# Kernel tuning notes

Hardware: AMD Instinct MI355X
Metric: run time of the kernel (lower is better)

The kernel has to match this reference:

```python
import jax, jax.numpy as jnp
import numpy as np

B, S, D, H = 2, 2048, 768, 12
DK = D // H


def setup_inputs() -> dict:
    key = jax.random.key(0)
    ks = jax.random.split(key, 10)
    sc = 0.02
    return {
        "k": jax.random.normal(ks[0], (B, S, D), jnp.float32),
        "q": jax.random.normal(ks[1], (B, S, D), jnp.float32),
        "v": jax.random.normal(ks[2], (B, S, D), jnp.float32),
        "mask": jnp.ones((B, 1, S, S), jnp.int32),
        "wq": jax.random.normal(ks[3], (D, D), jnp.float32) * sc,
        "bq": jnp.zeros((D,), jnp.float32),
        "wk": jax.random.normal(ks[4], (D, D), jnp.float32) * sc,
        "bk": jnp.zeros((D,), jnp.float32),
        "wv": jax.random.normal(ks[5], (D, D), jnp.float32) * sc,
        "bv": jnp.zeros((D,), jnp.float32),
        "wo": jax.random.normal(ks[6], (D, D), jnp.float32) * sc,
        "bo": jnp.zeros((D,), jnp.float32),
    }


def reference(k, q, v, mask, wq, bq, wk, bk, wv, bv, wo, bo):
    # Linear projections (torch Linear: x @ W^T + b)
    query = q @ wq.T + bq
    key_ = k @ wk.T + bk
    value = v @ wv.T + bv
    # [B,S,D] -> [B,H,S,DK]
    def split_heads(x):
        return x.reshape(B, S, H, DK).transpose(0, 2, 1, 3)
    Q, K, V = split_heads(query), split_heads(key_), split_heads(value)
    # NOTE: original masked_fill result is discarded -> mask is a no-op.
    scores = jnp.einsum("bhqd,bhkd->bhqk", Q, K) / jnp.sqrt(jnp.float32(DK))
    attn = jax.nn.softmax(scores, axis=-1)  # dropout p=0.0 -> identity
    out = jnp.einsum("bhqk,bhkd->bhqd", attn, V)
    out = out.transpose(0, 2, 1, 3).reshape(B, S, D)
    return out @ wo.T + bo
```

## Files before the change

### kernel.cpp

```cpp
#include <hip/hip_runtime.h>
#include <hip/hip_bf16.h>

#define B_  2
#define S_  2048
#define D_  768
#define H_  12
#define DK_ 64
#define NX_ (B_*S_*D_)
#define NW_ (D_*D_)

typedef __attribute__((ext_vector_type(8))) short  bf16x8;
typedef __attribute__((ext_vector_type(4))) float  f32x4;

__device__ __forceinline__ unsigned short f2bf(float f) {
    unsigned int u = __float_as_uint(f);
    u += 0x7fffu + ((u >> 16) & 1u);
    return (unsigned short)(u >> 16);
}

__device__ __forceinline__ void async_cp16(const unsigned short* g,
                                           const unsigned short* lds_uniform_base) {
    __builtin_amdgcn_global_load_lds(
        (const __attribute__((address_space(1))) unsigned int*)(uintptr_t)g,
        (__attribute__((address_space(3))) unsigned int*)(unsigned int)(uintptr_t)lds_uniform_base,
        16, 0, 0);
}

struct CvtArgs { const float* s[7]; unsigned short* d[7]; };

__global__ __launch_bounds__(256) void cvt_kernel(CvtArgs a) {
    const int reg = blockIdx.y;
    const int n = (reg < 3) ? NX_ : NW_;
    const long i = ((long)blockIdx.x * 256 + threadIdx.x) * 8;
    if (i >= n) return;
    const float4 f0 = *(const float4*)(a.s[reg] + i);
    const float4 f1 = *(const float4*)(a.s[reg] + i + 4);
    unsigned short o[8] = {f2bf(f0.x), f2bf(f0.y), f2bf(f0.z), f2bf(f0.w),
                           f2bf(f1.x), f2bf(f1.y), f2bf(f1.z), f2bf(f1.w)};
    *(uint4*)(a.d[reg] + i) = *(const uint4*)o;
}

struct QkvArgs {
    const unsigned short* A[3];
    const unsigned short* W[3];
    const float* bias[3];
    unsigned short* out[3];
};

__global__ __launch_bounds__(256) void gemm_qkv(QkvArgs args, int zoff) {
    __shared__ unsigned short smem[12288];
    unsigned short* As = smem;
    unsigned short* Bs = smem + 8192;

    const int t    = threadIdx.x;
    const int wave = t >> 6;
    const int lane = t & 63;
    const int l16  = lane & 15;
    const int quad = lane >> 4;
    const int m0   = blockIdx.x * 128;
    const int head = blockIdx.y;
    const int n0   = head * 64;
    const int zz   = blockIdx.z + zoff;

    const unsigned short* Ap = args.A[zz];
    const unsigned short* Wp = args.W[zz];

    f32x4 acc[2][4];
#pragma unroll
    for (int s = 0; s < 2; s++)
#pragma unroll
        for (int j = 0; j < 4; j++) acc[s][j] = (f32x4){0.f, 0.f, 0.f, 0.f};

    const int lrow = lane >> 3;
    const int lcg  = (lane & 7) * 8;

    for (int k0 = 0; k0 < D_; k0 += 64) {
#pragma unroll
        for (int i = 0; i < 4; i++) {
            const int chunk = wave * 4 + i;
            async_cp16(Ap + (long)(m0 + chunk * 8 + lrow) * D_ + k0 + lcg,
                       As + chunk * 512);
        }
#pragma unroll
        for (int i = 0; i < 2; i++) {
            const int chunk = wave * 2 + i;
            async_cp16(Wp + (long)(n0 + chunk * 8 + lrow) * D_ + k0 + lcg,
                       Bs + chunk * 512);
        }
        __syncthreads();
#pragma unroll
        for (int ks = 0; ks < 2; ks++) {
            bf16x8 af[2];
#pragma unroll
            for (int s = 0; s < 2; s++)
                af[s] = *(const bf16x8*)&As[(wave * 32 + s * 16 + l16) * 64 + ks * 32 + quad * 8];
#pragma unroll
            for (int j = 0; j < 4; j++) {
                const bf16x8 bf = *(const bf16x8*)&Bs[(j * 16 + l16) * 64 + ks * 32 + quad * 8];
#pragma unroll
                for (int s = 0; s < 2; s++)
                    acc[s][j] = __builtin_amdgcn_mfma_f32_16x16x32_bf16(af[s], bf, acc[s][j], 0, 0, 0);
            }
        }
        __syncthreads();
    }

    const int b     = m0 >> 11;
    const int sbase = m0 & (S_ - 1);
    float bv4[4];
#pragma unroll
    for (int j = 0; j < 4; j++) bv4[j] = args.bias[zz][n0 + j * 16 + l16];

    if (zz < 2) {
        unsigned short* Op = args.out[zz] + (long)(b * H_ + head) * S_ * DK_;
#pragma unroll
        for (int s = 0; s < 2; s++)
#pragma unroll
            for (int j = 0; j < 4; j++)
#pragma unroll
                for (int r = 0; r < 4; r++) {
                    const int srow = sbase + wave * 32 + s * 16 + quad * 4 + r;
                    Op[(long)srow * DK_ + j * 16 + l16] = f2bf(acc[s][j][r] + bv4[j]);
                }
    } else {
        unsigned short* Ls = smem;
#pragma unroll
        for (int s = 0; s < 2; s++)
#pragma unroll
            for (int j = 0; j < 4; j++)
#pragma unroll
                for (int r = 0; r < 4; r++)
                    Ls[(j * 16 + l16) * 136 + wave * 32 + s * 16 + quad * 4 + r] =
                        f2bf(acc[s][j][r] + bv4[j]);
        __syncthreads();
        const int dk = t >> 2;
        const int sg = (t & 3) * 32;
        uint4 w0 = *(const uint4*)&Ls[dk * 136 + sg];
        uint4 w1 = *(const uint4*)&Ls[dk * 136 + sg + 8];
        uint4 w2 = *(const uint4*)&Ls[dk * 136 + sg + 16];
        uint4 w3 = *(const uint4*)&Ls[dk * 136 + sg + 24];
        unsigned short* Op = args.out[2] +
            ((long)(b * H_ + head) * DK_ + dk) * S_ + sbase + sg;
        *(uint4*)(Op)      = w0;
        *(uint4*)(Op + 8)  = w1;
        *(uint4*)(Op + 16) = w2;
        *(uint4*)(Op + 24) = w3;
    }
}

__global__ __launch_bounds__(256) void attn_kernel(
    const unsigned short* __restrict__ Q, const unsigned short* __restrict__ K,
    const unsigned short* __restrict__ Vt, unsigned short* __restrict__ O)
{
    const int t    = threadIdx.x;
    const int wave = t >> 6;
    const int lane = t & 63;
    const int l16  = lane & 15;
    const int quad = lane >> 4;
    const int qtile = blockIdx.x;
    const int bh    = blockIdx.y;

    const unsigned short* Qp = Q  + (long)bh * S_ * DK_;
    const unsigned short* Kp = K  + (long)bh * S_ * DK_;
    const unsigned short* Vp = Vt + (long)bh * DK_ * S_;

    __shared__ unsigned short Ks[2][64 * 72];
    __shared__ unsigned short Vs[2][64 * 72];
    __shared__ unsigned short Ps[64 * 72];

    bf16x8 qfrag[2];
    {
        const long qoff = (long)(qtile * 64 + wave * 16 + l16) * DK_ + quad * 8;
        qfrag[0] = *(const bf16x8*)(Qp + qoff);
        qfrag[1] = *(const bf16x8*)(Qp + qoff + 32);
    }

    const int srow = t >> 3;
    const int scg  = (t & 7) * 8;
    uint4 kreg[2], vreg[2];

    kreg[0] = *(const uint4*)(Kp + (long)srow * DK_ + scg);
    kreg[1] = *(const uint4*)(Kp + (long)(srow + 32) * DK_ + scg);
    vreg[0] = *(const uint4*)(Vp + (long)srow * S_ + scg);
    vreg[1] = *(const uint4*)(Vp + (long)(srow + 32) * S_ + scg);
    *(uint4*)&Ks[0][srow * 72 + scg]        = kreg[0];
    *(uint4*)&Ks[0][(srow + 32) * 72 + scg] = kreg[1];
    *(uint4*)&Vs[0][srow * 72 + scg]        = vreg[0];
    *(uint4*)&Vs[0][(srow + 32) * 72 + scg] = vreg[1];
    __syncthreads();

    f32x4 oacc[4];
#pragma unroll
    for (int j = 0; j < 4; j++) oacc[j] = (f32x4){0.f, 0.f, 0.f, 0.f};
    float lsum[4] = {0.f, 0.f, 0.f, 0.f};

    const float C = 0.18033688011112042f;

    for (int it = 0; it < 32; ++it) {
        const int cur = it & 1;
        if (it < 31) {
            const int kv0 = (it + 1) * 64;
            kreg[0] = *(const uint4*)(Kp + (long)(kv0 + srow) * DK_ + scg);
            kreg[1] = *(const uint4*)(Kp + (long)(kv0 + srow + 32) * DK_ + scg);
            vreg[0] = *(const uint4*)(Vp + (long)srow * S_ + kv0 + scg);
            vreg[1] = *(const uint4*)(Vp + (long)(srow + 32) * S_ + kv0 + scg);
        }

        f32x4 sacc[4];
#pragma unroll
        for (int j = 0; j < 4; j++) sacc[j] = (f32x4){0.f, 0.f, 0.f, 0.f};
#pragma unroll
        for (int ks = 0; ks < 2; ks++)
#pragma unroll
            for (int j = 0; j < 4; j++) {
                const bf16x8 bf = *(const bf16x8*)&Ks[cur][(j * 16 + l16) * 72 + ks * 32 + quad * 8];
                sacc[j] = __builtin_amdgcn_mfma_f32_16x16x32_bf16(qfrag[ks], bf, sacc[j], 0, 0, 0);
            }

#pragma unroll
        for (int j = 0; j < 4; j++)
#pragma unroll
            for (int r = 0; r < 4; r++) {
                const float p = exp2f(sacc[j][r] * C);
                lsum[r] += p;
                Ps[(wave * 16 + quad * 4 + r) * 72 + j * 16 + l16] = f2bf(p);
            }

#pragma unroll
        for (int ks = 0; ks < 2; ks++) {
            const bf16x8 pf = *(const bf16x8*)&Ps[(wave * 16 + l16) * 72 + ks * 32 + quad * 8];
#pragma unroll
            for (int j = 0; j < 4; j++) {
                const bf16x8 vf = *(const bf16x8*)&Vs[cur][(j * 16 + l16) * 72 + ks * 32 + quad * 8];
                oacc[j] = __builtin_amdgcn_mfma_f32_16x16x32_bf16(pf, vf, oacc[j], 0, 0, 0);
            }
        }

        if (it < 31) {
            const int nxt = cur ^ 1;
            *(uint4*)&Ks[nxt][srow * 72 + scg]        = kreg[0];
            *(uint4*)&Ks[nxt][(srow + 32) * 72 + scg] = kreg[1];
            *(uint4*)&Vs[nxt][srow * 72 + scg]        = vreg[0];
            *(uint4*)&Vs[nxt][(srow + 32) * 72 + scg] = vreg[1];
        }
        __syncthreads();
    }

#pragma unroll
    for (int r = 0; r < 4; r++) {
#pragma unroll
        for (int off = 1; off < 16; off <<= 1)
            lsum[r] += __shfl_xor(lsum[r], off, 64);
        lsum[r] = 1.f / lsum[r];
    }

    const int b = bh / H_, h = bh % H_;
#pragma unroll
    for (int j = 0; j < 4; j++)
#pragma unroll
        for (int r = 0; r < 4; r++) {
            const int qrow = qtile * 64 + wave * 16 + quad * 4 + r;
            O[(long)(b * S_ + qrow) * D_ + h * DK_ + j * 16 + l16] =
                f2bf(oacc[j][r] * lsum[r]);
        }
}

__global__ __launch_bounds__(256) void gemm_out(
    const unsigned short* __restrict__ A, const unsigned short* __restrict__ W,
    const float* __restrict__ bias, float* __restrict__ Out)
{
    __shared__ unsigned short smem[12288];
    unsigned short* As = smem;
    unsigned short* Bs = smem + 8192;

    const int t    = threadIdx.x;
    const int wave = t >> 6;
    const int lane = t & 63;
    const int l16  = lane & 15;
    const int quad = lane >> 4;
    const int m0   = blockIdx.x * 128;
    const int n0   = blockIdx.y * 64;

    f32x4 acc[2][4];
#pragma unroll
    for (int s = 0; s < 2; s++)
#pragma unroll
        for (int j = 0; j < 4; j++) acc[s][j] = (f32x4){0.f, 0.f, 0.f, 0.f};

    const int lrow = lane >> 3;
    const int lcg  = (lane & 7) * 8;

    for (int k0 = 0; k0 < D_; k0 += 64) {
#pragma unroll
        for (int i = 0; i < 4; i++) {
            const int chunk = wave * 4 + i;
            async_cp16(A + (long)(m0 + chunk * 8 + lrow) * D_ + k0 + lcg,
                       As + chunk * 512);
        }
#pragma unroll
        for (int i = 0; i < 2; i++) {
            const int chunk = wave * 2 + i;
            async_cp16(W + (long)(n0 + chunk * 8 + lrow) * D_ + k0 + lcg,
                       Bs + chunk * 512);
        }
        __syncthreads();
#pragma unroll
        for (int ks = 0; ks < 2; ks++) {
            bf16x8 af[2];
#pragma unroll
            for (int s = 0; s < 2; s++)
                af[s] = *(const bf16x8*)&As[(wave * 32 + s * 16 + l16) * 64 + ks * 32 + quad * 8];
#pragma unroll
            for (int j = 0; j < 4; j++) {
                const bf16x8 bf = *(const bf16x8*)&Bs[(j * 16 + l16) * 64 + ks * 32 + quad * 8];
#pragma unroll
                for (int s = 0; s < 2; s++)
                    acc[s][j] = __builtin_amdgcn_mfma_f32_16x16x32_bf16(af[s], bf, acc[s][j], 0, 0, 0);
            }
        }
        __syncthreads();
    }

#pragma unroll
    for (int j = 0; j < 4; j++) {
        const float bv = bias[n0 + j * 16 + l16];
#pragma unroll
        for (int s = 0; s < 2; s++)
#pragma unroll
            for (int r = 0; r < 4; r++) {
                const int m = m0 + wave * 32 + s * 16 + quad * 4 + r;
                Out[(long)m * D_ + n0 + j * 16 + l16] = acc[s][j][r] + bv;
            }
    }
}

extern "C" void kernel_launch(void* const* d_in, const int* in_sizes, int n_in,
                              void* d_out, int out_size, void* d_ws, size_t ws_size,
                              hipStream_t stream) {
    const float* k_in = (const float*)d_in[0];
    const float* q_in = (const float*)d_in[1];
    const float* v_in = (const float*)d_in[2];
    const float* wq = (const float*)d_in[4];
    const float* bq = (const float*)d_in[5];
    const float* wk = (const float*)d_in[6];
    const float* bk = (const float*)d_in[7];
    const float* wv = (const float*)d_in[8];
    const float* bv = (const float*)d_in[9];
    const float* wo = (const float*)d_in[10];
    const float* bo = (const float*)d_in[11];

    unsigned short* ws = (unsigned short*)d_ws;
    unsigned short* R0 = ws;
    unsigned short* R1 = ws + 1ll * NX_;
    unsigned short* R2 = ws + 2ll * NX_;

    const size_t need_fused = (6ull * NX_ + 4ull * NW_) * 2;
    const bool fused = ws_size >= need_fused;

    unsigned short *Qb, *Kb, *Vtp, *Ao, *Wc;
    if (fused) {
        Qb  = ws + 3ll * NX_;
        Kb  = ws + 4ll * NX_;
        Vtp = ws + 5ll * NX_;
        Ao  = R0;
        Wc  = ws + 6ll * NX_;
    } else {
        Qb  = ws + 3ll * NX_;
        Kb  = R0;
        Vtp = R1;
        Ao  = R2;
        Wc  = ws + 4ll * NX_;
    }
    unsigned short* W0 = Wc;
    unsigned short* W1 = Wc + 1ll * NW_;
    unsigned short* W2 = Wc + 2ll * NW_;
    unsigned short* W3 = Wc + 3ll * NW_;

    CvtArgs ca;
    ca.s[0] = q_in; ca.s[1] = k_in; ca.s[2] = v_in;
    ca.s[3] = wq;   ca.s[4] = wk;   ca.s[5] = wv;  ca.s[6] = wo;
    ca.d[0] = R0;   ca.d[1] = R1;   ca.d[2] = R2;
    ca.d[3] = W0;   ca.d[4] = W1;   ca.d[5] = W2;  ca.d[6] = W3;
    cvt_kernel<<<dim3(NX_ / 2048, 7), 256, 0, stream>>>(ca);

    QkvArgs qa;
    qa.A[0] = R0;  qa.A[1] = R1;  qa.A[2] = R2;
    qa.W[0] = W0;  qa.W[1] = W1;  qa.W[2] = W2;
    qa.bias[0] = bq; qa.bias[1] = bk; qa.bias[2] = bv;
    qa.out[0] = Qb; qa.out[1] = Kb; qa.out[2] = Vtp;

    if (fused) {
        gemm_qkv<<<dim3(32, 12, 3), 256, 0, stream>>>(qa, 0);
    } else {
        gemm_qkv<<<dim3(32, 12, 1), 256, 0, stream>>>(qa, 0);
        gemm_qkv<<<dim3(32, 12, 1), 256, 0, stream>>>(qa, 1);
        gemm_qkv<<<dim3(32, 12, 1), 256, 0, stream>>>(qa, 2);
    }

    attn_kernel<<<dim3(S_ / 64, B_ * H_), 256, 0, stream>>>(Qb, Kb, Vtp, Ao);
    gemm_out<<<dim3(32, 12), 256, 0, stream>>>(Ao, W3, bo, (float*)d_out);
}
```

Baseline: 234.9 us.

## Fuse input conversion into QKV GEMM, split-KV attention, swizzled weights, retile GEMMs

Drops the separate fp32-to-bf16 conversion of the activations and converts them inside the QKV GEMM as they are loaded. Only the weights are still pre-converted, now into an XOR-swizzled LDS-friendly layout. The QKV GEMM moves to 128x128 tiles with a 2x2 wave layout and staged coalesced epilogues. Attention processes 128 query rows per block and splits the KV range in two, with a combine kernel that merges the partial sums. The output GEMM uses smaller 64x64 tiles for more blocks. These changes remove a full pass over the activations and add parallelism, at the cost of extra fp32 partial traffic and an extra launch.

After: 241.4 us. 2.8% more time.

```diff
diff --git a/kernel.cpp b/kernel.cpp
--- a/kernel.cpp
+++ b/kernel.cpp
@@ -8,6 +8,7 @@
 #define DK_ 64
 #define NX_ (B_*S_*D_)
 #define NW_ (D_*D_)
+#define NR_ (B_*H_*S_)
 
 typedef __attribute__((ext_vector_type(8))) short  bf16x8;
 typedef __attribute__((ext_vector_type(4))) float  f32x4;
@@ -26,29 +27,33 @@
         16, 0, 0);
 }
 
-struct CvtArgs { const float* s[7]; unsigned short* d[7]; };
-
-__global__ __launch_bounds__(256) void cvt_kernel(CvtArgs a) {
-    const int reg = blockIdx.y;
-    const int n = (reg < 3) ? NX_ : NW_;
-    const long i = ((long)blockIdx.x * 256 + threadIdx.x) * 8;
-    if (i >= n) return;
-    const float4 f0 = *(const float4*)(a.s[reg] + i);
-    const float4 f1 = *(const float4*)(a.s[reg] + i + 4);
+__global__ __launch_bounds__(256) void cvt_w(const float* __restrict__ w0,
+                                             const float* __restrict__ w1,
+                                             const float* __restrict__ w2,
+                                             const float* __restrict__ w3,
+                                             unsigned short* __restrict__ dst) {
+    const float* src[4] = {w0, w1, w2, w3};
+    const int widx = blockIdx.y;
+    const int idx  = blockIdx.x * 256 + threadIdx.x;
+    const int n = idx / 96;
+    const int g = idx % 96;
+    const float4 f0 = *(const float4*)(src[widx] + (long)n * D_ + g * 8);
+    const float4 f1 = *(const float4*)(src[widx] + (long)n * D_ + g * 8 + 4);
     unsigned short o[8] = {f2bf(f0.x), f2bf(f0.y), f2bf(f0.z), f2bf(f0.w),
                            f2bf(f1.x), f2bf(f1.y), f2bf(f1.z), f2bf(f1.w)};
-    *(uint4*)(a.d[reg] + i) = *(const uint4*)o;
+    const int kdst = (g >> 3) * 64 + (((g & 7) ^ (n & 7)) * 8);
+    *(uint4*)(dst + (long)widx * NW_ + (long)n * D_ + kdst) = *(const uint4*)o;
 }
 
 struct QkvArgs {
-    const unsigned short* A[3];
-    const unsigned short* W[3];
+    const float* X[3];
     const float* bias[3];
     unsigned short* out[3];
 };
 
-__global__ __launch_bounds__(256) void gemm_qkv(QkvArgs args, int zoff) {
-    __shared__ unsigned short smem[12288];
+__global__ __launch_bounds__(256, 2) void gemm_qkv(QkvArgs args,
+                                                   const unsigned short* __restrict__ Wsw) {
+    __shared__ __align__(16) unsigned short smem[17408];
     unsigned short* As = smem;
     unsigned short* Bs = smem + 8192;
 
@@ -57,100 +62,126 @@
     const int lane = t & 63;
     const int l16  = lane & 15;
     const int quad = lane >> 4;
+    const int wm   = wave >> 1, wn = wave & 1;
     const int m0   = blockIdx.x * 128;
-    const int head = blockIdx.y;
-    const int n0   = head * 64;
-    const int zz   = blockIdx.z + zoff;
-
-    const unsigned short* Ap = args.A[zz];
-    const unsigned short* Wp = args.W[zz];
-
-    f32x4 acc[2][4];
-#pragma unroll
-    for (int s = 0; s < 2; s++)
+    const int zz   = blockIdx.y / 6;
+    const int nb   = blockIdx.y % 6;
+    const int n0   = nb * 128;
+
+    const float* Xp = args.X[zz];
+    const unsigned short* Wp = Wsw + (long)zz * NW_;
+
+    f32x4 acc[4][4];
+#pragma unroll
+    for (int s = 0; s < 4; s++)
 #pragma unroll
         for (int j = 0; j < 4; j++) acc[s][j] = (f32x4){0.f, 0.f, 0.f, 0.f};
 
-    const int lrow = lane >> 3;
-    const int lcg  = (lane & 7) * 8;
+    const int arow = t >> 3;
+    const int acg  = t & 7;
+    const int brow = lane >> 3;
+    const int bcg  = lane & 7;
 
     for (int k0 = 0; k0 < D_; k0 += 64) {
+        __syncthreads();
 #pragma unroll
         for (int i = 0; i < 4; i++) {
             const int chunk = wave * 4 + i;
-            async_cp16(Ap + (long)(m0 + chunk * 8 + lrow) * D_ + k0 + lcg,
-                       As + chunk * 512);
-        }
-#pragma unroll
-        for (int i = 0; i < 2; i++) {
-            const int chunk = wave * 2 + i;
-            async_cp16(Wp + (long)(n0 + chunk * 8 + lrow) * D_ + k0 + lcg,
+            async_cp16(Wp + (long)(n0 + chunk * 8 + brow) * D_ + k0 + bcg * 8,
                        Bs + chunk * 512);
         }
+#pragma unroll
+        for (int p = 0; p < 4; p++) {
+            const int r = p * 32 + arow;
+            const float4 f0 = *(const float4*)(Xp + (long)(m0 + r) * D_ + k0 + acg * 8);
+            const float4 f1 = *(const float4*)(Xp + (long)(m0 + r) * D_ + k0 + acg * 8 + 4);
+            unsigned short o[8] = {f2bf(f0.x), f2bf(f0.y), f2bf(f0.z), f2bf(f0.w),
+                                   f2bf(f1.x), f2bf(f1.y), f2bf(f1.z), f2bf(f1.w)};
+            *(uint4*)(As + r * 64 + ((acg ^ (r & 7)) * 8)) = *(const uint4*)o;
+        }
         __syncthreads();
 #pragma unroll
         for (int ks = 0; ks < 2; ks++) {
-            bf16x8 af[2];
-#pragma unroll
-            for (int s = 0; s < 2; s++)
-                af[s] = *(const bf16x8*)&As[(wave * 32 + s * 16 + l16) * 64 + ks * 32 + quad * 8];
+            const int cg = ks * 4 + quad;
+            bf16x8 af[4], bf[4];
+#pragma unroll
+            for (int s = 0; s < 4; s++) {
+                const int r = wm * 64 + s * 16 + l16;
+                af[s] = *(const bf16x8*)&As[r * 64 + ((cg ^ (r & 7)) * 8)];
+            }
 #pragma unroll
             for (int j = 0; j < 4; j++) {
-                const bf16x8 bf = *(const bf16x8*)&Bs[(j * 16 + l16) * 64 + ks * 32 + quad * 8];
-#pragma unroll
-                for (int s = 0; s < 2; s++)
-                    acc[s][j] = __builtin_amdgcn_mfma_f32_16x16x32_bf16(af[s], bf, acc[s][j], 0, 0, 0);
-            }
-        }
-        __syncthreads();
-    }
+                const int r = wn * 64 + j * 16 + l16;
+                bf[j] = *(const bf16x8*)&Bs[r * 64 + ((cg ^ (r & 7)) * 8)];
+            }
+#pragma unroll
+            for (int s = 0; s < 4; s++)
+#pragma unroll
+                for (int j = 0; j < 4; j++)
+                    acc[s][j] = __builtin_amdgcn_mfma_f32_16x16x32_bf16(af[s], bf[j], acc[s][j], 0, 0, 0);
+        }
+    }
+    __syncthreads();
 
     const int b     = m0 >> 11;
     const int sbase = m0 & (S_ - 1);
-    float bv4[4];
-#pragma unroll
-    for (int j = 0; j < 4; j++) bv4[j] = args.bias[zz][n0 + j * 16 + l16];
+    float bv[4];
+#pragma unroll
+    for (int j = 0; j < 4; j++) bv[j] = args.bias[zz][n0 + wn * 64 + j * 16 + l16];
 
     if (zz < 2) {
-        unsigned short* Op = args.out[zz] + (long)(b * H_ + head) * S_ * DK_;
-#pragma unroll
-        for (int s = 0; s < 2; s++)
+        unsigned short* Ls = smem;
+#pragma unroll
+        for (int s = 0; s < 4; s++)
 #pragma unroll
             for (int j = 0; j < 4; j++)
 #pragma unroll
-                for (int r = 0; r < 4; r++) {
-                    const int srow = sbase + wave * 32 + s * 16 + quad * 4 + r;
-                    Op[(long)srow * DK_ + j * 16 + l16] = f2bf(acc[s][j][r] + bv4[j]);
-                }
+                for (int r = 0; r < 4; r++)
+                    Ls[(wm * 64 + s * 16 + quad * 4 + r) * 136 + wn * 64 + j * 16 + l16] =
+                        f2bf(acc[s][j][r] + bv[j]);
+        __syncthreads();
+        const int row  = t >> 1;
+        const int half = t & 1;
+        unsigned short* Op = args.out[zz];
+#pragma unroll
+        for (int i = 0; i < 8; i++) {
+            const int col  = half * 64 + i * 8;
+            const int head = nb * 2 + half;
+            const uint4 v = *(const uint4*)&Ls[row * 136 + col];
+            *(uint4*)(Op + ((long)(b * H_ + head) * S_ + sbase + row) * DK_ + (col & 63)) = v;
+        }
     } else {
         unsigned short* Ls = smem;
 #pragma unroll
-        for (int s = 0; s < 2; s++)
+        for (int s = 0; s < 4; s++)
 #pragma unroll
             for (int j = 0; j < 4; j++)
 #pragma unroll
-                for (int r = 0; r < 4; r++)
-                    Ls[(j * 16 + l16) * 136 + wave * 32 + s * 16 + quad * 4 + r] =
-                        f2bf(acc[s][j][r] + bv4[j]);
-        __syncthreads();
-        const int dk = t >> 2;
-        const int sg = (t & 3) * 32;
-        uint4 w0 = *(const uint4*)&Ls[dk * 136 + sg];
-        uint4 w1 = *(const uint4*)&Ls[dk * 136 + sg + 8];
-        uint4 w2 = *(const uint4*)&Ls[dk * 136 + sg + 16];
-        uint4 w3 = *(const uint4*)&Ls[dk * 136 + sg + 24];
-        unsigned short* Op = args.out[2] +
-            ((long)(b * H_ + head) * DK_ + dk) * S_ + sbase + sg;
-        *(uint4*)(Op)      = w0;
-        *(uint4*)(Op + 8)  = w1;
-        *(uint4*)(Op + 16) = w2;
-        *(uint4*)(Op + 24) = w3;
-    }
-}
-
-__global__ __launch_bounds__(256) void attn_kernel(
+                for (int r = 0; r < 4; r++) {
+                    const int dk  = j * 16 + l16;
+                    const int pos = wm * 64 + (quad * 4 + r) * 4 + s;
+                    Ls[wn * 8704 + dk * 136 + pos] = f2bf(acc[s][j][r] + bv[j]);
+                }
+        __syncthreads();
+        const int rowIdx = t >> 1;
+        const int hh = rowIdx >> 6, dk = rowIdx & 63;
+        const int half = t & 1;
+        unsigned short* Op = args.out[2];
+#pragma unroll
+        for (int i = 0; i < 8; i++) {
+            const int col = half * 64 + i * 8;
+            const uint4 v = *(const uint4*)&Ls[hh * 8704 + dk * 136 + col];
+            const int head = nb * 2 + hh;
+            *(uint4*)(Op + ((long)(b * H_ + head) * DK_ + dk) * S_ + sbase + col) = v;
+        }
+    }
+}
+
+__global__ __launch_bounds__(256, 3) void attn_kernel(
     const unsigned short* __restrict__ Q, const unsigned short* __restrict__ K,
-    const unsigned short* __restrict__ Vt, unsigned short* __restrict__ O)
+    const unsigned short* __restrict__ Vt,
+    float* __restrict__ Opart, float* __restrict__ Lp,
+    unsigned short* __restrict__ Ao, int kvlen, int direct)
 {
     const int t    = threadIdx.x;
     const int wave = t >> 6;
@@ -159,177 +190,238 @@
     const int quad = lane >> 4;
     const int qtile = blockIdx.x;
     const int bh    = blockIdx.y;
+    const int z     = blockIdx.z;
+    const int kvbase = z * kvlen;
+    const int NIT    = kvlen >> 6;
 
     const unsigned short* Qp = Q  + (long)bh * S_ * DK_;
     const unsigned short* Kp = K  + (long)bh * S_ * DK_;
     const unsigned short* Vp = Vt + (long)bh * DK_ * S_;
 
-    __shared__ unsigned short Ks[2][64 * 72];
-    __shared__ unsigned short Vs[2][64 * 72];
-    __shared__ unsigned short Ps[64 * 72];
-
-    bf16x8 qfrag[2];
+    __shared__ __align__(16) unsigned short smem[18432];
+    unsigned short* Ks = smem;
+    unsigned short* Vs = smem + 4608;
+    unsigned short* Ps = smem + 9216;
+
+    bf16x8 qfrag[2][2];
+#pragma unroll
+    for (int st = 0; st < 2; st++) {
+        const long qoff = (long)(qtile * 128 + wave * 32 + st * 16 + l16) * DK_ + quad * 8;
+        qfrag[st][0] = *(const bf16x8*)(Qp + qoff);
+        qfrag[st][1] = *(const bf16x8*)(Qp + qoff + 32);
+    }
+
+    const int srow = t >> 2;
+    const int scg  = (t & 3) * 16;
+    uint4 kreg[2], vreg[2];
     {
-        const long qoff = (long)(qtile * 64 + wave * 16 + l16) * DK_ + quad * 8;
-        qfrag[0] = *(const bf16x8*)(Qp + qoff);
-        qfrag[1] = *(const bf16x8*)(Qp + qoff + 32);
-    }
-
-    const int srow = t >> 3;
-    const int scg  = (t & 7) * 8;
-    uint4 kreg[2], vreg[2];
-
-    kreg[0] = *(const uint4*)(Kp + (long)srow * DK_ + scg);
-    kreg[1] = *(const uint4*)(Kp + (long)(srow + 32) * DK_ + scg);
-    vreg[0] = *(const uint4*)(Vp + (long)srow * S_ + scg);
-    vreg[1] = *(const uint4*)(Vp + (long)(srow + 32) * S_ + scg);
-    *(uint4*)&Ks[0][srow * 72 + scg]        = kreg[0];
-    *(uint4*)&Ks[0][(srow + 32) * 72 + scg] = kreg[1];
-    *(uint4*)&Vs[0][srow * 72 + scg]        = vreg[0];
-    *(uint4*)&Vs[0][(srow + 32) * 72 + scg] = vreg[1];
-    __syncthreads();
-
-    f32x4 oacc[4];
-#pragma unroll
-    for (int j = 0; j < 4; j++) oacc[j] = (f32x4){0.f, 0.f, 0.f, 0.f};
-    float lsum[4] = {0.f, 0.f, 0.f, 0.f};
+        const unsigned short* gk = Kp + (long)(kvbase + srow) * DK_ + scg;
+        const unsigned short* gv = Vp + (long)srow * S_ + kvbase + scg;
+        kreg[0] = *(const uint4*)gk;  kreg[1] = *(const uint4*)(gk + 8);
+        vreg[0] = *(const uint4*)gv;  vreg[1] = *(const uint4*)(gv + 8);
+    }
+
+    f32x4 oacc[2][4];
+#pragma unroll
+    for (int st = 0; st < 2; st++)
+#pragma unroll
+        for (int j = 0; j < 4; j++) oacc[st][j] = (f32x4){0.f, 0.f, 0.f, 0.f};
+    float lsum[2][4] = {{0.f,0.f,0.f,0.f},{0.f,0.f,0.f,0.f}};
 
     const float C = 0.18033688011112042f;
 
-    for (int it = 0; it < 32; ++it) {
-        const int cur = it & 1;
-        if (it < 31) {
-            const int kv0 = (it + 1) * 64;
-            kreg[0] = *(const uint4*)(Kp + (long)(kv0 + srow) * DK_ + scg);
-            kreg[1] = *(const uint4*)(Kp + (long)(kv0 + srow + 32) * DK_ + scg);
-            vreg[0] = *(const uint4*)(Vp + (long)srow * S_ + kv0 + scg);
-            vreg[1] = *(const uint4*)(Vp + (long)(srow + 32) * S_ + kv0 + scg);
-        }
-
-        f32x4 sacc[4];
-#pragma unroll
-        for (int j = 0; j < 4; j++) sacc[j] = (f32x4){0.f, 0.f, 0.f, 0.f};
+    for (int it = 0; it < NIT; ++it) {
+        __syncthreads();
+        *(uint4*)&Ks[srow * 72 + scg]     = kreg[0];
+        *(uint4*)&Ks[srow * 72 + scg + 8] = kreg[1];
+        *(uint4*)&Vs[srow * 72 + scg]     = vreg[0];
+        *(uint4*)&Vs[srow * 72 + scg + 8] = vreg[1];
+        __syncthreads();
+        if (it + 1 < NIT) {
+            const int kv0 = kvbase + (it + 1) * 64;
+            const unsigned short* gk = Kp + (long)(kv0 + srow) * DK_ + scg;
+            const unsigned short* gv = Vp + (long)srow * S_ + kv0 + scg;
+            kreg[0] = *(const uint4*)gk;  kreg[1] = *(const uint4*)(gk + 8);
+            vreg[0] = *(const uint4*)gv;  vreg[1] = *(const uint4*)(gv + 8);
+        }
+
+        f32x4 sacc[2][4];
+#pragma unroll
+        for (int st = 0; st < 2; st++)
+#pragma unroll
+            for (int j = 0; j < 4; j++) sacc[st][j] = (f32x4){0.f, 0.f, 0.f, 0.f};
 #pragma unroll
         for (int ks = 0; ks < 2; ks++)
 #pragma unroll
             for (int j = 0; j < 4; j++) {
-                const bf16x8 bf = *(const bf16x8*)&Ks[cur][(j * 16 + l16) * 72 + ks * 32 + quad * 8];
-                sacc[j] = __builtin_amdgcn_mfma_f32_16x16x32_bf16(qfrag[ks], bf, sacc[j], 0, 0, 0);
-            }
-
-#pragma unroll
-        for (int j = 0; j < 4; j++)
+                const bf16x8 bf = *(const bf16x8*)&Ks[(j * 16 + l16) * 72 + ks * 32 + quad * 8];
+#pragma unroll
+                for (int st = 0; st < 2; st++)
+                    sacc[st][j] = __builtin_amdgcn_mfma_f32_16x16x32_bf16(qfrag[st][ks], bf, sacc[st][j], 0, 0, 0);
+            }
+
+#pragma unroll
+        for (int st = 0; st < 2; st++)
 #pragma unroll
             for (int r = 0; r < 4; r++) {
-                const float p = exp2f(sacc[j][r] * C);
-                lsum[r] += p;
-                Ps[(wave * 16 + quad * 4 + r) * 72 + j * 16 + l16] = f2bf(p);
-            }
-
-#pragma unroll
-        for (int ks = 0; ks < 2; ks++) {
-            const bf16x8 pf = *(const bf16x8*)&Ps[(wave * 16 + l16) * 72 + ks * 32 + quad * 8];
-#pragma unroll
-            for (int j = 0; j < 4; j++) {
-                const bf16x8 vf = *(const bf16x8*)&Vs[cur][(j * 16 + l16) * 72 + ks * 32 + quad * 8];
-                oacc[j] = __builtin_amdgcn_mfma_f32_16x16x32_bf16(pf, vf, oacc[j], 0, 0, 0);
-            }
-        }
-
-        if (it < 31) {
-            const int nxt = cur ^ 1;
-            *(uint4*)&Ks[nxt][srow * 72 + scg]        = kreg[0];
-            *(uint4*)&Ks[nxt][(srow + 32) * 72 + scg] = kreg[1];
-            *(uint4*)&Vs[nxt][srow * 72 + scg]        = vreg[0];
-            *(uint4*)&Vs[nxt][(srow + 32) * 72 + scg] = vreg[1];
-        }
-        __syncthreads();
-    }
-
-#pragma unroll
-    for (int r = 0; r < 4; r++) {
-#pragma unroll
-        for (int off = 1; off < 16; off <<= 1)
-            lsum[r] += __shfl_xor(lsum[r], off, 64);
-        lsum[r] = 1.f / lsum[r];
-    }
-
+                unsigned short p4[4];
+#pragma unroll
+                for (int j = 0; j < 4; j++) {
+                    const float p = exp2f(sacc[st][j][r] * C);
+                    lsum[st][r] += p;
+                    p4[j] = f2bf(p);
+                }
+                const int row = wave * 32 + st * 16 + quad * 4 + r;
+                *(uint2*)&Ps[row * 72 + l16 * 4] = *(const uint2*)p4;
+            }
+
+#pragma unroll
+        for (int st = 0; st < 2; st++)
+#pragma unroll
+            for (int ks = 0; ks < 2; ks++) {
+                const bf16x8 pf = *(const bf16x8*)&Ps[(wave * 32 + st * 16 + l16) * 72 + ks * 32 + quad * 8];
+#pragma unroll
+                for (int j = 0; j < 4; j++) {
+                    const bf16x8 vf = *(const bf16x8*)&Vs[(j * 16 + l16) * 72 + ks * 32 + quad * 8];
+                    oacc[st][j] = __builtin_amdgcn_mfma_f32_16x16x32_bf16(pf, vf, oacc[st][j], 0, 0, 0);
+                }
+            }
+    }
+
+#pragma unroll
+    for (int st = 0; st < 2; st++)
+#pragma unroll
+        for (int r = 0; r < 4; r++)
+#pragma unroll
+            for (int off = 1; off < 16; off <<= 1)
+                lsum[st][r] += __shfl_xor(lsum[st][r], off, 64);
+
+    if (direct) {
+        const int b = bh / H_, h = bh % H_;
+#pragma unroll
+        for (int st = 0; st < 2; st++)
+#pragma unroll
+            for (int r = 0; r < 4; r++) {
+                const float inv = 1.f / lsum[st][r];
+                const int qrow = qtile * 128 + wave * 32 + st * 16 + quad * 4 + r;
+#pragma unroll
+                for (int j = 0; j < 4; j++)
+                    Ao[(long)(b * S_ + qrow) * D_ + h * DK_ + j * 16 + l16] =
+                        f2bf(oacc[st][j][r] * inv);
+            }
+    } else {
+        float* Op = Opart + (long)z * NX_ + (long)bh * S_ * DK_;
+        float* Lq = Lp + (long)z * NR_ + (long)bh * S_;
+#pragma unroll
+        for (int st = 0; st < 2; st++)
+#pragma unroll
+            for (int r = 0; r < 4; r++) {
+                const int qrow = qtile * 128 + wave * 32 + st * 16 + quad * 4 + r;
+#pragma unroll
+                for (int j = 0; j < 4; j++)
+                    Op[(long)qrow * DK_ + j * 16 + l16] = oacc[st][j][r];
+                if (l16 == 0) Lq[qrow] = lsum[st][r];
+            }
+    }
+}
+
+__global__ __launch_bounds__(256) void combine_kernel(
+    const float* __restrict__ Opart, const float* __restrict__ Lp,
+    unsigned short* __restrict__ Ao)
+{
+    const long i = ((long)blockIdx.x * 256 + threadIdx.x) * 8;
+    const int row = (int)(i >> 6);
+    const float l = Lp[row] + Lp[NR_ + row];
+    const float inv = 1.f / l;
+    const float4 a0 = *(const float4*)(Opart + i);
+    const float4 a1 = *(const float4*)(Opart + i + 4);
+    const float4 b0 = *(const float4*)(Opart + NX_ + i);
+    const float4 b1 = *(const float4*)(Opart + NX_ + i + 4);
+    unsigned short o[8] = {
+        f2bf((a0.x + b0.x) * inv), f2bf((a0.y + b0.y) * inv),
+        f2bf((a0.z + b0.z) * inv), f2bf((a0.w + b0.w) * inv),
+        f2bf((a1.x + b1.x) * inv), f2bf((a1.y + b1.y) * inv),
+        f2bf((a1.z + b1.z) * inv), f2bf((a1.w + b1.w) * inv)};
+    const int bh = row >> 11, s = row & (S_ - 1), dk0 = (int)(i & 63);
     const int b = bh / H_, h = bh % H_;
-#pragma unroll
-    for (int j = 0; j < 4; j++)
-#pragma unroll
-        for (int r = 0; r < 4; r++) {
-            const int qrow = qtile * 64 + wave * 16 + quad * 4 + r;
-            O[(long)(b * S_ + qrow) * D_ + h * DK_ + j * 16 + l16] =
-                f2bf(oacc[j][r] * lsum[r]);
-        }
-}
-
-__global__ __launch_bounds__(256) void gemm_out(
-    const unsigned short* __restrict__ A, const unsigned short* __restrict__ W,
+    *(uint4*)(Ao + (long)(b * S_ + s) * D_ + h * DK_ + dk0) = *(const uint4*)o;
+}
+
+__global__ __launch_bounds__(256, 2) void gemm_out(
+    const unsigned short* __restrict__ A, const unsigned short* __restrict__ Wsw,
     const float* __restrict__ bias, float* __restrict__ Out)
 {
-    __shared__ unsigned short smem[12288];
+    __shared__ __align__(16) unsigned short smem[8192];
     unsigned short* As = smem;
-    unsigned short* Bs = smem + 8192;
+    unsigned short* Bs = smem + 4096;
 
     const int t    = threadIdx.x;
     const int wave = t >> 6;
     const int lane = t & 63;
     const int l16  = lane & 15;
     const int quad = lane >> 4;
-    const int m0   = blockIdx.x * 128;
+    const int wm   = wave >> 1, wn = wave & 1;
+    const int m0   = blockIdx.x * 64;
     const int n0   = blockIdx.y * 64;
 
-    f32x4 acc[2][4];
+    f32x4 acc[2][2];
 #pragma unroll
     for (int s = 0; s < 2; s++)
 #pragma unroll
-        for (int j = 0; j < 4; j++) acc[s][j] = (f32x4){0.f, 0.f, 0.f, 0.f};
-
-    const int lrow = lane >> 3;
-    const int lcg  = (lane & 7) * 8;
+        for (int j = 0; j < 2; j++) acc[s][j] = (f32x4){0.f, 0.f, 0.f, 0.f};
+
+    const int arow = t >> 2;
+    const int acg2 = (t & 3) * 2;
+    const int brow = lane >> 3;
+    const int bcg  = lane & 7;
 
     for (int k0 = 0; k0 < D_; k0 += 64) {
-#pragma unroll
-        for (int i = 0; i < 4; i++) {
-            const int chunk = wave * 4 + i;
-            async_cp16(A + (long)(m0 + chunk * 8 + lrow) * D_ + k0 + lcg,
-                       As + chunk * 512);
-        }
+        __syncthreads();
 #pragma unroll
         for (int i = 0; i < 2; i++) {
             const int chunk = wave * 2 + i;
-            async_cp16(W + (long)(n0 + chunk * 8 + lrow) * D_ + k0 + lcg,
+            async_cp16(Wsw + (long)(n0 + chunk * 8 + brow) * D_ + k0 + bcg * 8,
                        Bs + chunk * 512);
         }
+        {
+            const uint4 v0 = *(const uint4*)(A + (long)(m0 + arow) * D_ + k0 + acg2 * 8);
+            const uint4 v1 = *(const uint4*)(A + (long)(m0 + arow) * D_ + k0 + acg2 * 8 + 8);
+            *(uint4*)(As + arow * 64 + ((acg2 ^ (arow & 7)) * 8))       = v0;
+            *(uint4*)(As + arow * 64 + (((acg2 + 1) ^ (arow & 7)) * 8)) = v1;
+        }
         __syncthreads();
 #pragma unroll
         for (int ks = 0; ks < 2; ks++) {
-            bf16x8 af[2];
+            const int cg = ks * 4 + quad;
+            bf16x8 af[2], bf[2];
+#pragma unroll
+            for (int s = 0; s < 2; s++) {
+                const int r = wm * 32 + s * 16 + l16;
+                af[s] = *(const bf16x8*)&As[r * 64 + ((cg ^ (r & 7)) * 8)];
+            }
+#pragma unroll
+            for (int j = 0; j < 2; j++) {
+                const int r = wn * 32 + j * 16 + l16;
+                bf[j] = *(const bf16x8*)&Bs[r * 64 + ((cg ^ (r & 7)) * 8)];
+            }
 #pragma unroll
             for (int s = 0; s < 2; s++)
-                af[s] = *(const bf16x8*)&As[(wave * 32 + s * 16 + l16) * 64 + ks * 32 + quad * 8];
-#pragma unroll
-            for (int j = 0; j < 4; j++) {
-                const bf16x8 bf = *(const bf16x8*)&Bs[(j * 16 + l16) * 64 + ks * 32 + quad * 8];
-#pragma unroll
-                for (int s = 0; s < 2; s++)
-                    acc[s][j] = __builtin_amdgcn_mfma_f32_16x16x32_bf16(af[s], bf, acc[s][j], 0, 0, 0);
-            }
-        }
-        __syncthreads();
-    }
-
-#pragma unroll
-    for (int j = 0; j < 4; j++) {
-        const float bv = bias[n0 + j * 16 + l16];
+#pragma unroll
+                for (int j = 0; j < 2; j++)
+                    acc[s][j] = __builtin_amdgcn_mfma_f32_16x16x32_bf16(af[s], bf[j], acc[s][j], 0, 0, 0);
+        }
+    }
+
+#pragma unroll
+    for (int j = 0; j < 2; j++) {
+        const int n = n0 + wn * 32 + j * 16 + l16;
+        const float bv = bias[n];
 #pragma unroll
         for (int s = 0; s < 2; s++)
 #pragma unroll
             for (int r = 0; r < 4; r++) {
-                const int m = m0 + wave * 32 + s * 16 + quad * 4 + r;
-                Out[(long)m * D_ + n0 + j * 16 + l16] = acc[s][j][r] + bv;
+                const int m = m0 + wm * 32 + s * 16 + quad * 4 + r;
+                Out[(long)m * D_ + n] = acc[s][j][r] + bv;
             }
     }
 }
@@ -350,53 +442,35 @@
     const float* bo = (const float*)d_in[11];
 
     unsigned short* ws = (unsigned short*)d_ws;
-    unsigned short* R0 = ws;
-    unsigned short* R1 = ws + 1ll * NX_;
-    unsigned short* R2 = ws + 2ll * NX_;
-
-    const size_t need_fused = (6ull * NX_ + 4ull * NW_) * 2;
-    const bool fused = ws_size >= need_fused;
-
-    unsigned short *Qb, *Kb, *Vtp, *Ao, *Wc;
-    if (fused) {
-        Qb  = ws + 3ll * NX_;
-        Kb  = ws + 4ll * NX_;
-        Vtp = ws + 5ll * NX_;
-        Ao  = R0;
-        Wc  = ws + 6ll * NX_;
+    unsigned short* Wsw = ws;
+    unsigned short* Qb  = ws + 4ll * NW_;
+    unsigned short* Kb  = Qb + (long)NX_;
+    unsigned short* Vt  = Kb + (long)NX_;
+
+    const size_t need_split = (4ull * NW_ + 3ull * NX_) * 2 + 2ull * NX_ * 4 + 2ull * NR_ * 4;
+    const bool split = ws_size >= need_split;
+
+    float* Opart = (float*)(Vt + (long)NX_);
+    float* Lp    = Opart + 2ll * NX_;
+    unsigned short* Ao = split ? Qb
+                               : (unsigned short*)(Vt + (long)NX_);
+
+    cvt_w<<<dim3(288, 4), 256, 0, stream>>>(wq, wk, wv, wo, Wsw);
+
+    QkvArgs qa;
+    qa.X[0] = q_in; qa.X[1] = k_in; qa.X[2] = v_in;
+    qa.bias[0] = bq; qa.bias[1] = bk; qa.bias[2] = bv;
+    qa.out[0] = Qb; qa.out[1] = Kb; qa.out[2] = Vt;
+    gemm_qkv<<<dim3(32, 18), 256, 0, stream>>>(qa, Wsw);
+
+    if (split) {
+        attn_kernel<<<dim3(S_ / 128, B_ * H_, 2), 256, 0, stream>>>(
+            Qb, Kb, Vt, Opart, Lp, nullptr, S_ / 2, 0);
+        combine_kernel<<<dim3(NX_ / 2048), 256, 0, stream>>>(Opart, Lp, Ao);
     } else {
-        Qb  = ws + 3ll * NX_;
-        Kb  = R0;
-        Vtp = R1;
-        Ao  = R2;
-        Wc  = ws + 4ll * NX_;
-    }
-    unsigned short* W0 = Wc;
-    unsigned short* W1 = Wc + 1ll * NW_;
-    unsigned short* W2 = Wc + 2ll * NW_;
-    unsigned short* W3 = Wc + 3ll * NW_;
-
-    CvtArgs ca;
-    ca.s[0] = q_in; ca.s[1] = k_in; ca.s[2] = v_in;
-    ca.s[3] = wq;   ca.s[4] = wk;   ca.s[5] = wv;  ca.s[6] = wo;
-    ca.d[0] = R0;   ca.d[1] = R1;   ca.d[2] = R2;
-    ca.d[3] = W0;   ca.d[4] = W1;   ca.d[5] = W2;  ca.d[6] = W3;
-    cvt_kernel<<<dim3(NX_ / 2048, 7), 256, 0, stream>>>(ca);
-
-    QkvArgs qa;
-    qa.A[0] = R0;  qa.A[1] = R1;  qa.A[2] = R2;
-    qa.W[0] = W0;  qa.W[1] = W1;  qa.W[2] = W2;
-    qa.bias[0] = bq; qa.bias[1] = bk; qa.bias[2] = bv;
-    qa.out[0] = Qb; qa.out[1] = Kb; qa.out[2] = Vtp;
-
-    if (fused) {
-        gemm_qkv<<<dim3(32, 12, 3), 256, 0, stream>>>(qa, 0);
-    } else {
-        gemm_qkv<<<dim3(32, 12, 1), 256, 0, stream>>>(qa, 0);
-        gemm_qkv<<<dim3(32, 12, 1), 256, 0, stream>>>(qa, 1);
-        gemm_qkv<<<dim3(32, 12, 1), 256, 0, stream>>>(qa, 2);
-    }
-
-    attn_kernel<<<dim3(S_ / 64, B_ * H_), 256, 0, stream>>>(Qb, Kb, Vtp, Ao);
-    gemm_out<<<dim3(32, 12), 256, 0, stream>>>(Ao, W3, bo, (float*)d_out);
-}
+        attn_kernel<<<dim3(S_ / 128, B_ * H_, 1), 256, 0, stream>>>(
+            Qb, Kb, Vt, nullptr, nullptr, Ao, S_, 1);
+    }
+
+    gemm_out<<<dim3(64, 12), 256, 0, stream>>>(Ao, Wsw + 3ll * NW_, bo, (float*)d_out);
+}
```
